# Kernel optimization log

Hardware: AMD Instinct MI355X
Metric: run time of the kernel (lower is better)

The kernel has to match this reference:

```python
import jax, jax.numpy as jnp
import numpy as np


def _attention(v, W, static_hidden, dec_hidden):
    # static_hidden: [B,N,H], dec_hidden: [B,1,H], v: [1,1,H], W: [1,H,2H]
    hidden = jnp.concatenate(
        [static_hidden, jnp.broadcast_to(dec_hidden, static_hidden.shape)], axis=2
    )  # [B,N,2H]
    e = jnp.tanh(jnp.einsum('bnk,hk->bnh', hidden, W[0]))  # W @ hidden^T, done row-wise
    scores = jnp.einsum('bnh,h->bn', e, v[0, 0])  # [B,N]
    return jax.nn.softmax(scores, axis=1)[:, None, :]  # [B,1,N]


def _gru_step(x, h, w_ih, w_hh, b_ih, b_hh):
    # x: [B,H] input, h: [B,H] prev hidden; PyTorch gate order: r | z | n
    gx = x @ w_ih.T + b_ih  # [B,3H]
    gh = h @ w_hh.T + b_hh  # [B,3H]
    H = h.shape[-1]
    r = jax.nn.sigmoid(gx[:, :H] + gh[:, :H])
    z = jax.nn.sigmoid(gx[:, H:2 * H] + gh[:, H:2 * H])
    n = jnp.tanh(gx[:, 2 * H:] + r * gh[:, 2 * H:])
    return (1.0 - z) * n + z * h


def _pointer_scores(v, W, static_hidden, context, state_embedding):
    # energy = cat(static, context, state_emb) -> [B,N,3H]
    energy = jnp.concatenate(
        [static_hidden,
         jnp.broadcast_to(context, static_hidden.shape),
         jnp.broadcast_to(state_embedding, static_hidden.shape)], axis=2)
    e = jnp.tanh(jnp.einsum('bnk,hk->bnh', energy, W[0]))  # [B,N,H]
    return jnp.einsum('bnh,h->bn', e, v[0, 0])  # [B,N]


def setup_inputs() -> dict:
    key = jax.random.key(0)
    B, N, H = 128, 512, 512
    ks = jax.random.split(key, 16)
    s = 0.05
    return {
        'static_hidden': jax.random.normal(ks[0], (B, N, H), jnp.float32),
        'state_embedding': jax.random.normal(ks[1], (B, 1, H), jnp.float32),
        'decoder_hidden': jax.random.normal(ks[2], (B, 1, H), jnp.float32),
        'target_hidden': jax.random.normal(ks[3], (B, 1, H), jnp.float32),
        'last_hh': jax.random.normal(ks[4], (1, B, H), jnp.float32),
        # Pointer params (note: target branch of the original reuses self.v/self.W)
        'ptr_v': jax.random.normal(ks[5], (1, 1, H), jnp.float32) * s,
        'ptr_W': jax.random.normal(ks[6], (1, H, 3 * H), jnp.float32) * s,
        # encoder attention params
        'enc_v': jax.random.normal(ks[7], (1, 1, H), jnp.float32) * s,
        'enc_W': jax.random.normal(ks[8], (1, H, 2 * H), jnp.float32) * s,
        # target attention params
        'tgt_v': jax.random.normal(ks[9], (1, 1, H), jnp.float32) * s,
        'tgt_W': jax.random.normal(ks[10], (1, H, 2 * H), jnp.float32) * s,
        # GRU (single layer) params
        'gru_w_ih': jax.random.normal(ks[11], (3 * H, H), jnp.float32) * s,
        'gru_w_hh': jax.random.normal(ks[12], (3 * H, H), jnp.float32) * s,
        'gru_b_ih': jax.random.normal(ks[13], (3 * H,), jnp.float32) * s,
        'gru_b_hh': jax.random.normal(ks[14], (3 * H,), jnp.float32) * s,
    }


def reference(static_hidden, state_embedding, decoder_hidden, target_hidden, last_hh,
              ptr_v, ptr_W, enc_v, enc_W, tgt_v, tgt_W,
              gru_w_ih, gru_w_hh, gru_b_ih, gru_b_hh):
    # GRU over seq len 1 (batch_first); dropout layers are identity (eval mode)
    h_new = _gru_step(decoder_hidden[:, 0, :], last_hh[0], gru_w_ih, gru_w_hh, gru_b_ih, gru_b_hh)
    rnn_out = h_new[:, None, :]          # [B,1,H]
    new_last_hh = h_new[None]            # [1,B,H]

    # encoder attention + context
    enc_attn = _attention(enc_v, enc_W, static_hidden, rnn_out)   # [B,1,N]
    context = jnp.matmul(enc_attn, static_hidden)                 # [B,1,H]
    probs = _pointer_scores(ptr_v, ptr_W, static_hidden, context, state_embedding)

    # target attention + context (original reuses self.v/self.W for scoring)
    tgt_attn = _attention(tgt_v, tgt_W, static_hidden, target_hidden)
    context_t = jnp.matmul(tgt_attn, static_hidden)
    probs_target = _pointer_scores(ptr_v, ptr_W, static_hidden, context_t, state_embedding)

    probs = 5.0 * probs + probs_target
    return (probs, new_last_hh)
```

## Files before the change

### kernel.cpp

```cpp
#include <hip/hip_runtime.h>
#include <math.h>

#define B 128
#define N 512
#define H 512

typedef __attribute__((ext_vector_type(8))) short short8;
typedef __attribute__((ext_vector_type(4))) float floatx4;

typedef const __attribute__((address_space(1))) unsigned int* gas_t;
typedef __attribute__((address_space(3))) unsigned int* las_t;

__device__ __forceinline__ void gl16(const void* g, void* l){
    __builtin_amdgcn_global_load_lds((gas_t)g, (las_t)l, 16, 0, 0);
}

__device__ __forceinline__ float sigmoidf_(float x){ return 1.0f/(1.0f+__expf(-x)); }

__device__ __forceinline__ float fast_tanh(float x){
    float t = __expf(-2.0f*fabsf(x));
    float r = __fdividef(1.0f - t, 1.0f + t);
    return copysignf(r, x);
}

__device__ __forceinline__ unsigned f2bf1(float f){
    unsigned u = __float_as_uint(f);
    u += 0x7FFFu + ((u>>16)&1u);
    return u>>16;
}
__device__ __forceinline__ unsigned pk2(float a, float b){
    return f2bf1(a) | (f2bf1(b)<<16);
}

__global__ __launch_bounds__(256) void k_cast_all(
    const float* __restrict__ encW, const float* __restrict__ tgtW,
    const float* __restrict__ ptrW, const float* __restrict__ wih,
    const float* __restrict__ whh,
    const float* __restrict__ dec, const float* __restrict__ lhh,
    const float* __restrict__ tgt, const float* __restrict__ sem,
    const float* __restrict__ A,
    unsigned short* __restrict__ We_s, unsigned short* __restrict__ Wt_s,
    unsigned short* __restrict__ Wp_s, unsigned short* __restrict__ We_d,
    unsigned short* __restrict__ Wt_d, unsigned short* __restrict__ Wp_c,
    unsigned short* __restrict__ Wp_e, unsigned short* __restrict__ Wih_b,
    unsigned short* __restrict__ Whh_b,
    unsigned short* __restrict__ Xbf, unsigned short* __restrict__ Hbf,
    unsigned short* __restrict__ Tbf, unsigned short* __restrict__ Sbf,
    unsigned short* __restrict__ Abf)
{
    int r = blockIdx.x, t = threadIdx.x;
    if (r < 6656){
        const float* src; unsigned short* dst; int pitch, off, row;
        if (r < 512)      { src=encW; dst=We_s; pitch=2*H; off=0;   row=r; }
        else if (r<1024)  { src=tgtW; dst=Wt_s; pitch=2*H; off=0;   row=r-512; }
        else if (r<1536)  { src=ptrW; dst=Wp_s; pitch=3*H; off=0;   row=r-1024; }
// ... 131 lines not shown
            short8 af[4], bg[4];
            #pragma unroll
            for (int i=0;i<4;++i){
                int m = wy*64 + i*16 + li;
                int kb = (ks*4 + quad) ^ (m&7);
                af[i] = *(const short8*)&As[m*64 + kb*8];
            }
            #pragma unroll
            for (int j=0;j<4;++j){
                int h = wx*64 + j*16 + li;
                int kb = (ks*4 + quad) ^ (h&7);
                bg[j] = *(const short8*)&Bs[h*64 + kb*8];
            }
            #pragma unroll
            for (int i=0;i<4;++i)
              #pragma unroll
              for (int j=0;j<4;++j)
                acc[i][j] = __builtin_amdgcn_mfma_f32_16x16x32_bf16(af[i], bg[j], acc[i][j], 0,0,0);
        }
        __syncthreads();
    }
    #pragma unroll
    for (int i=0;i<4;++i)
      #pragma unroll
      for (int j=0;j<4;++j)
        #pragma unroll
        for (int rg=0;rg<4;++rg){
            int m = wy*64 + i*16 + quad*4 + rg;
            int n = wx*64 + j*16 + li;
            C[(size_t)m*ldc + n] = acc[i][j][rg];
        }
}

__global__ __launch_bounds__(256,2) void k_gru_gemm(
    const unsigned short* __restrict__ Xbf, const unsigned short* __restrict__ Hbf,
    const unsigned short* __restrict__ Wih_b, const unsigned short* __restrict__ Whh_b,
    float* __restrict__ gx, float* __restrict__ gh)
{
    int blk = blockIdx.x;
    int mat = blk / 12, nt = blk % 12;
    const unsigned short* Ab = mat ? Hbf : Xbf;
    const unsigned short* Bb = (mat ? Whh_b : Wih_b) + (size_t)nt*128*512;
    float* C = (mat ? gh : gx) + nt*128;
    gemm128_tile(Ab, Bb, C, 3*H);
}

__global__ __launch_bounds__(256) void k_gru_gate(const float* __restrict__ gx,
    const float* __restrict__ gh, const float* __restrict__ lhh,
    const float* __restrict__ bih, const float* __restrict__ bhh,
    float* __restrict__ out_hh, unsigned short* __restrict__ hnew_bf)
{
    int idx = blockIdx.x*256 + threadIdx.x;
    int b = idx >> 9, k = idx & 511;
    const float* gxb = gx + (size_t)b*(3*H);
    const float* ghb = gh + (size_t)b*(3*H);
    float r = sigmoidf_(gxb[k]     + bih[k]     + ghb[k]     + bhh[k]);
    float z = sigmoidf_(gxb[H+k]   + bih[H+k]   + ghb[H+k]   + bhh[H+k]);
    float n = tanhf(gxb[2*H+k] + bih[2*H+k] + r*(ghb[2*H+k] + bhh[2*H+k]));
    float h = (1.f-z)*n + z*lhh[idx];
    out_hh[idx] = h;
    hnew_bf[idx] = (unsigned short)f2bf1(h);
}

__global__ __launch_bounds__(256,2) void k_bias_gemm(
    const unsigned short* __restrict__ HNbf, const unsigned short* __restrict__ Tbf,
    const unsigned short* __restrict__ Sbf,
    const unsigned short* __restrict__ We_d, const unsigned short* __restrict__ Wt_d,
    const unsigned short* __restrict__ Wp_e,
    float* __restrict__ d_enc, float* __restrict__ d_tgt, float* __restrict__ d_se)
{
    int blk = blockIdx.x;
    int mat = blk >> 2, nt = blk & 3;
    const unsigned short* Ab = mat==0 ? HNbf : mat==1 ? Tbf : Sbf;
    const unsigned short* Bb = (mat==0 ? We_d : mat==1 ? Wt_d : Wp_e) + (size_t)nt*128*512;
    float* C = (mat==0 ? d_enc : mat==1 ? d_tgt : d_se) + nt*128;
    gemm128_tile(Ab, Bb, C, H);
}

__global__ __launch_bounds__(256,2) void k_dptr_gemm(
    const float* __restrict__ ctx, const float* __restrict__ ctxt,
    const unsigned short* __restrict__ Wp_c,
    float* __restrict__ d_pe, float* __restrict__ d_pt)
{
    int blk = blockIdx.x;
    int mat = blk >> 2, nt = blk & 3;
    const float* Af = mat ? ctxt : ctx;
    const unsigned short* Bb = Wp_c + (size_t)nt*128*512;
    float* C = (mat ? d_pt : d_pe) + nt*128;
    gemm128_tile_f32A(Af, Bb, C, H);
}

template<bool BF16A>
__global__ __launch_bounds__(256,2) void k_scores_fused(
    const float* __restrict__ Af, const unsigned short* __restrict__ Abf,
    const unsigned short* __restrict__ We, const unsigned short* __restrict__ Wt,
    const float* __restrict__ d_enc, const float* __restrict__ d_tgt,
    const float* __restrict__ enc_v, const float* __restrict__ tgt_v,
    float* __restrict__ sc_e, float* __restrict__ sc_t)
{
    __shared__ __align__(16) unsigned short As[128*64];
    __shared__ __align__(16) unsigned short Be[128*64];
    __shared__ __align__(16) unsigned short Bt[128*64];
    int blk = blockIdx.x;
    int b = blk >> 4; int nt = (blk >> 2) & 3; int ht = blk & 3;
    int n0 = nt*128, hb = ht*128;
    int t = threadIdx.x;
    int lane = t & 63, wave = t >> 6;
    int wy = wave >> 1, wx = wave & 1;
    int li = lane & 15, quad = lane >> 4;

    floatx4 acc_e[4][4], acc_t[4][4];
    #pragma unroll
    for (int i=0;i<4;++i)
      #pragma unroll
      for (int j=0;j<4;++j){ acc_e[i][j]=(floatx4)(0.0f); acc_t[i][j]=(floatx4)(0.0f); }

    for (int kt=0; kt<8; ++kt){
        int k0 = kt*64;
        #pragma unroll
        for (int c=0;c<4;++c){
            int s = c*256 + t;
            int row = s >> 3;
            int kb = (s & 7) ^ (row & 7);
            if constexpr (BF16A){
                gl16(&Abf[(size_t)(b*N+n0+row)*H + k0 + kb*8], &As[(size_t)s*8]);
            } else {
                const float* src = Af + (size_t)(b*N+n0+row)*H + k0 + kb*8;
                float4 lo = *(const float4*)src;
                float4 hi = *(const float4*)(src+4);
                uint4 p;
                p.x = pk2(lo.x,lo.y); p.y = pk2(lo.z,lo.w);
                p.z = pk2(hi.x,hi.y); p.w = pk2(hi.z,hi.w);
                *(uint4*)&As[(size_t)s*8] = p;
            }
            gl16(&We[(size_t)(hb+row)*H + k0 + kb*8], &Be[(size_t)s*8]);
            gl16(&Wt[(size_t)(hb+row)*H + k0 + kb*8], &Bt[(size_t)s*8]);
        }
        __syncthreads();
        #pragma unroll
        for (int ks=0;ks<2;++ks){
            short8 af[4], be[4], bt[4];
            #pragma unroll
            for (int i=0;i<4;++i){
                int m = wy*64 + i*16 + li;
                int kb = (ks*4 + quad) ^ (m&7);
                af[i] = *(const short8*)&As[m*64 + kb*8];
            }
            #pragma unroll
            for (int j=0;j<4;++j){
                int h = wx*64 + j*16 + li;
                int kb = (ks*4 + quad) ^ (h&7);
                be[j] = *(const short8*)&Be[h*64 + kb*8];
                bt[j] = *(const short8*)&Bt[h*64 + kb*8];
            }
            #pragma unroll
            for (int i=0;i<4;++i)
              #pragma unroll
              for (int j=0;j<4;++j){
                acc_e[i][j] = __builtin_amdgcn_mfma_f32_16x16x32_bf16(af[i], be[j], acc_e[i][j], 0,0,0);
                acc_t[i][j] = __builtin_amdgcn_mfma_f32_16x16x32_bf16(af[i], bt[j], acc_t[i][j], 0,0,0);
              }
        }
        __syncthreads();
    }
    float nse[4][4], nst[4][4];
    #pragma unroll
    for (int i=0;i<4;++i)
      #pragma unroll
      for (int rg=0;rg<4;++rg){ nse[i][rg]=0.f; nst[i][rg]=0.f; }
    #pragma unroll
    for (int j=0;j<4;++j){
        int hm = hb + wx*64 + j*16 + li;
        float dje = d_enc[b*H+hm], vje = enc_v[hm];
        float djt = d_tgt[b*H+hm], vjt = tgt_v[hm];
        #pragma unroll
        for (int i=0;i<4;++i)
          #pragma unroll
          for (int rg=0;rg<4;++rg){
            nse[i][rg] += vje * fast_tanh(acc_e[i][j][rg] + dje);
            nst[i][rg] += vjt * fast_tanh(acc_t[i][j][rg] + djt);
          }
    }
    #pragma unroll
    for (int off=1; off<16; off<<=1)
      #pragma unroll
      for (int i=0;i<4;++i)
        #pragma unroll
        for (int rg=0;rg<4;++rg){
          nse[i][rg] += __shfl_xor(nse[i][rg], off);
          nst[i][rg] += __shfl_xor(nst[i][rg], off);
        }
    if (li==0){
        #pragma unroll
        for (int i=0;i<4;++i)
          #pragma unroll
          for (int rg=0;rg<4;++rg){
            atomicAdd(&sc_e[b*N + n0 + wy*64 + i*16 + quad*4 + rg], nse[i][rg]);
            atomicAdd(&sc_t[b*N + n0 + wy*64 + i*16 + quad*4 + rg], nst[i][rg]);
          }
    }
}

__global__ __launch_bounds__(256) void k_softmax(const float* __restrict__ sc_e,
    const float* __restrict__ sc_t, float* __restrict__ w_e, float* __restrict__ w_t)
{
    __shared__ float buf[256];
    int b = blockIdx.x, t = threadIdx.x;
    float x0 = sc_e[b*N+t], x1 = sc_e[b*N+t+256];
    float m = fmaxf(x0,x1);
    buf[t]=m; __syncthreads();
    for (int s2=128;s2>0;s2>>=1){ if(t<s2) buf[t]=fmaxf(buf[t],buf[t+s2]); __syncthreads(); }
    m = buf[0]; __syncthreads();
    float e0 = __expf(x0-m), e1 = __expf(x1-m);
    buf[t]=e0+e1; __syncthreads();
    for (int s2=128;s2>0;s2>>=1){ if(t<s2) buf[t]+=buf[t+s2]; __syncthreads(); }
    float inv = 1.0f/buf[0]; __syncthreads();
    w_e[b*N+t]=e0*inv; w_e[b*N+t+256]=e1*inv;
    x0 = sc_t[b*N+t]; x1 = sc_t[b*N+t+256];
    m = fmaxf(x0,x1);
    buf[t]=m; __syncthreads();
    for (int s2=128;s2>0;s2>>=1){ if(t<s2) buf[t]=fmaxf(buf[t],buf[t+s2]); __syncthreads(); }
    m = buf[0]; __syncthreads();
    e0 = __expf(x0-m); e1 = __expf(x1-m);
    buf[t]=e0+e1; __syncthreads();
    for (int s2=128;s2>0;s2>>=1){ if(t<s2) buf[t]+=buf[t+s2]; __syncthreads(); }
    inv = 1.0f/buf[0];
    w_t[b*N+t]=e0*inv; w_t[b*N+t+256]=e1*inv;
}

__global__ __launch_bounds__(256) void k_context_bf16(const unsigned short* __restrict__ Abf,
    const float* __restrict__ w_e, const float* __restrict__ w_t,
    float* __restrict__ ctx, float* __restrict__ ctxt)
{
    __shared__ float we[64], wt[64];
    int b = blockIdx.x >> 3, c = blockIdx.x & 7, t = threadIdx.x;
    int n0 = c*64;
    if (t < 64){ we[t]=w_e[b*N+n0+t]; wt[t]=w_t[b*N+n0+t]; }
    __syncthreads();
    float ae0=0.f, ae1=0.f, at0=0.f, at1=0.f;
    for (int n=0;n<64;++n){
        unsigned u = *(const unsigned*)&Abf[(size_t)(b*N+n0+n)*H + 2*t];
        float lo = __uint_as_float(u<<16);
        float hi = __uint_as_float(u & 0xFFFF0000u);
        float e = we[n], g = wt[n];
        ae0 += e*lo; ae1 += e*hi; at0 += g*lo; at1 += g*hi;
    }
    atomicAdd(&ctx[b*H+2*t],   ae0); atomicAdd(&ctx[b*H+2*t+1],  ae1);
    atomicAdd(&ctxt[b*H+2*t],  at0); atomicAdd(&ctxt[b*H+2*t+1], at1);
}

__global__ __launch_bounds__(256) void k_context(const float* __restrict__ A,
    const float* __restrict__ w_e, const float* __restrict__ w_t,
    float* __restrict__ ctx, float* __restrict__ ctxt)
{
    __shared__ float we[128], wt[128];
    int b = blockIdx.x >> 2, c = blockIdx.x & 3, t = threadIdx.x;
    int n0 = c*128;
    if (t < 128){ we[t]=w_e[b*N+n0+t]; wt[t]=w_t[b*N+n0+t]; }
    __syncthreads();
    float ae0=0.f, ae1=0.f, at0=0.f, at1=0.f;
    for (int n=0;n<128;++n){
        const float* ar = A + (size_t)(b*N + n0 + n)*H;
        float a0 = ar[t], a1 = ar[t+256];
        ae0 += we[n]*a0; ae1 += we[n]*a1;
        at0 += wt[n]*a0; at1 += wt[n]*a1;
    }
    atomicAdd(&ctx[b*H+t],      ae0); atomicAdd(&ctx[b*H+t+256],  ae1);
    atomicAdd(&ctxt[b*H+t],     at0); atomicAdd(&ctxt[b*H+t+256], at1);
}

template<bool BF16A>
__global__ __launch_bounds__(256,2) void k_probs_mfma(
    const float* __restrict__ Af, const unsigned short* __restrict__ Abf,
    const unsigned short* __restrict__ Wp,
    const float* __restrict__ d_pe, const float* __restrict__ d_pt,
    const float* __restrict__ d_se,
    const float* __restrict__ ptr_v, float* __restrict__ probs)
{
    __shared__ __align__(16) unsigned short As[128*64];
    __shared__ __align__(16) unsigned short Bs[128*64];
    int blk = blockIdx.x;
    int b = blk >> 4; int nt = (blk >> 2) & 3; int ht = blk & 3;
    int n0 = nt*128, hb = ht*128;

    int t = threadIdx.x;
    int lane = t & 63, wave = t >> 6;
    int wy = wave >> 1, wx = wave & 1;
    int li = lane & 15, quad = lane >> 4;

    floatx4 acc[4][4];
    #pragma unroll
    for (int i=0;i<4;++i)
      #pragma unroll
      for (int j=0;j<4;++j) acc[i][j] = (floatx4)(0.0f);

    for (int kt=0; kt<8; ++kt){
        int k0 = kt*64;
        #pragma unroll
        for (int c=0;c<4;++c){
            int s = c*256 + t;
            int row = s >> 3;
            int kb = (s & 7) ^ (row & 7);
            if constexpr (BF16A){
                gl16(&Abf[(size_t)(b*N+n0+row)*H + k0 + kb*8], &As[(size_t)s*8]);
            } else {
                const float* src = Af + (size_t)(b*N+n0+row)*H + k0 + kb*8;
                float4 lo = *(const float4*)src;
                float4 hi = *(const float4*)(src+4);
                uint4 p;
                p.x = pk2(lo.x,lo.y); p.y = pk2(lo.z,lo.w);
                p.z = pk2(hi.x,hi.y); p.w = pk2(hi.z,hi.w);
                *(uint4*)&As[(size_t)s*8] = p;
            }
            gl16(&Wp[(size_t)(hb+row)*H + k0 + kb*8], &Bs[(size_t)s*8]);
        }
        __syncthreads();
        #pragma unroll
        for (int ks=0;ks<2;++ks){
            short8 af[4], bg[4];
            #pragma unroll
            for (int i=0;i<4;++i){
                int m = wy*64 + i*16 + li;
                int kb = (ks*4 + quad) ^ (m&7);
                af[i] = *(const short8*)&As[m*64 + kb*8];
            }
            #pragma unroll
            for (int j=0;j<4;++j){
                int h = wx*64 + j*16 + li;
                int kb = (ks*4 + quad) ^ (h&7);
                bg[j] = *(const short8*)&Bs[h*64 + kb*8];
            }
            #pragma unroll
            for (int i=0;i<4;++i)
              #pragma unroll
              for (int j=0;j<4;++j)
                acc[i][j] = __builtin_amdgcn_mfma_f32_16x16x32_bf16(af[i], bg[j], acc[i][j], 0,0,0);
        }
        __syncthreads();
    }
    float nsum[4][4];
    #pragma unroll
    for (int i=0;i<4;++i){ nsum[i][0]=0.f;nsum[i][1]=0.f;nsum[i][2]=0.f;nsum[i][3]=0.f; }
    #pragma unroll
    for (int j=0;j<4;++j){
        int hm = hb + wx*64 + j*16 + li;
        float se = d_se[b*H + hm];
        float de = d_pe[b*H + hm] + se;
        float dt = d_pt[b*H + hm] + se;
        float vj = ptr_v[hm];
        #pragma unroll
        for (int i=0;i<4;++i)
          #pragma unroll
          for (int rg=0;rg<4;++rg){
            float s = acc[i][j][rg];
            nsum[i][rg] += vj * (5.0f*fast_tanh(s + de) + fast_tanh(s + dt));
          }
    }
    #pragma unroll
    for (int off=1; off<16; off<<=1)
      #pragma unroll
      for (int i=0;i<4;++i)
        #pragma unroll
        for (int rg=0;rg<4;++rg)
          nsum[i][rg] += __shfl_xor(nsum[i][rg], off);
    if (li==0){
        #pragma unroll
        for (int i=0;i<4;++i)
          #pragma unroll
          for (int rg=0;rg<4;++rg)
            atomicAdd(&probs[b*N + n0 + wy*64 + i*16 + quad*4 + rg], nsum[i][rg]);
    }
}
// ... 1 lines not shown
extern "C" void kernel_launch(void* const* d_in, const int* in_sizes, int n_in,
                              void* d_out, int out_size, void* d_ws, size_t ws_size,
                              hipStream_t stream)
{
    (void)in_sizes; (void)n_in; (void)out_size;
    const float* A    = (const float*)d_in[0];
    const float* sem  = (const float*)d_in[1];
    const float* dec  = (const float*)d_in[2];
    const float* tgt  = (const float*)d_in[3];
    const float* lhh  = (const float*)d_in[4];
    const float* ptrv = (const float*)d_in[5];
    const float* ptrW = (const float*)d_in[6];
    const float* encv = (const float*)d_in[7];
    const float* encW = (const float*)d_in[8];
    const float* tgtv = (const float*)d_in[9];
    const float* tgtW = (const float*)d_in[10];
    const float* wih  = (const float*)d_in[11];
    const float* whh  = (const float*)d_in[12];
    const float* bih  = (const float*)d_in[13];
    const float* bhh  = (const float*)d_in[14];

    float* probs_out = (float*)d_out;
    float* hh_out    = (float*)d_out + B*N;

    float* ws = (float*)d_ws;
    const size_t S = (size_t)B*H;
    float* d_enc = ws;
    float* d_tgt = ws + S;
    float* d_se  = ws + 2*S;
    float* sc_e  = ws + 3*S;
    float* sc_t  = ws + 4*S;
    float* ctx   = ws + 5*S;
    float* ctxt  = ws + 6*S;
    float* w_e   = ws + 7*S;
    float* w_t   = ws + 8*S;
    float* d_pe  = ws + 9*S;
    float* d_pt  = ws + 10*S;
    float* gx    = ws + 11*S;
    float* gh    = ws + 14*S;
    unsigned short* bfb  = (unsigned short*)(ws + 17*S);
    const size_t WH = (size_t)H*H;
    const size_t WG = (size_t)3*H*H;
    unsigned short* We_s  = bfb;
    unsigned short* Wt_s  = We_s + WH;
    unsigned short* Wp_s  = Wt_s + WH;
    unsigned short* We_d  = Wp_s + WH;
    unsigned short* Wt_d  = We_d + WH;
    unsigned short* Wp_c  = Wt_d + WH;
    unsigned short* Wp_e  = Wp_c + WH;
    unsigned short* Wih_b = Wp_e + WH;
    unsigned short* Whh_b = Wih_b + WG;
    unsigned short* Xbf   = Whh_b + WG;
    unsigned short* Hbf   = Xbf + S;
    unsigned short* Tbf   = Hbf + S;
    unsigned short* Sbf   = Tbf + S;
    unsigned short* HNbf  = Sbf + S;
    unsigned short* Abf   = HNbf + S;

    const size_t need_full = 17*S*sizeof(float)
        + (7*WH + 2*WG + 5*S + (size_t)B*N*H) * sizeof(unsigned short);
    const bool big = ws_size >= need_full;

    hipMemsetAsync(sc_e, 0, 4*S*sizeof(float), stream);
    hipMemsetAsync(probs_out, 0, (size_t)B*N*sizeof(float), stream);

    int castA_blocks = big ? (int)(((size_t)B*N*H)/(256*8)) : 0;
    k_cast_all<<<6784 + castA_blocks, 256, 0, stream>>>(encW, tgtW, ptrW, wih, whh,
        dec, lhh, tgt, sem, A,
        We_s, Wt_s, Wp_s, We_d, Wt_d, Wp_c, Wp_e, Wih_b, Whh_b,
        Xbf, Hbf, Tbf, Sbf, Abf);

    k_gru_gemm<<<24, 256, 0, stream>>>(Xbf, Hbf, Wih_b, Whh_b, gx, gh);
    k_gru_gate<<<256, 256, 0, stream>>>(gx, gh, lhh, bih, bhh, hh_out, HNbf);
    k_bias_gemm<<<12, 256, 0, stream>>>(HNbf, Tbf, Sbf, We_d, Wt_d, Wp_e, d_enc, d_tgt, d_se);

    if (big)
        k_scores_fused<true ><<<2048, 256, 0, stream>>>(A, Abf, We_s, Wt_s, d_enc, d_tgt, encv, tgtv, sc_e, sc_t);
    else
        k_scores_fused<false><<<2048, 256, 0, stream>>>(A, Abf, We_s, Wt_s, d_enc, d_tgt, encv, tgtv, sc_e, sc_t);
    k_softmax<<<B, 256, 0, stream>>>(sc_e, sc_t, w_e, w_t);
    if (big)
        k_context_bf16<<<B*8, 256, 0, stream>>>(Abf, w_e, w_t, ctx, ctxt);
    else
        k_context<<<B*4, 256, 0, stream>>>(A, w_e, w_t, ctx, ctxt);

    k_dptr_gemm<<<8, 256, 0, stream>>>(ctx, ctxt, Wp_c, d_pe, d_pt);

    if (big)
        k_probs_mfma<true ><<<2048, 256, 0, stream>>>(A, Abf, Wp_s, d_pe, d_pt, d_se, ptrv, probs_out);
    else
        k_probs_mfma<false><<<2048, 256, 0, stream>>>(A, Abf, Wp_s, d_pe, d_pt, d_se, ptrv, probs_out);
}
```

Before: 472.9 us.

## Load MFMA fragments directly from global, use rational tanh, merge bias GEMMs

The two large MFMA kernels (scores and pointer probs) no longer stage A and W tiles through LDS with barriers. Each lane now loads its bf16 fragments straight from global memory and the k-loop is fully unrolled, which removes the LDS traffic and syncs but depends on L1/L2 for reuse across waves. fast_tanh becomes a clamped Padé rational approximation in place of an exp plus divide. The target and state bias GEMMs move into the GRU GEMM launch, since they do not depend on the GRU output, leaving a smaller separate launch for the encoder bias.

```diff
diff --git a/kernel.cpp b/kernel.cpp
--- a/kernel.cpp
+++ b/kernel.cpp
@@ -18,9 +18,11 @@
 __device__ __forceinline__ float sigmoidf_(float x){ return 1.0f/(1.0f+__expf(-x)); }
 
 __device__ __forceinline__ float fast_tanh(float x){
-    float t = __expf(-2.0f*fabsf(x));
-    float r = __fdividef(1.0f - t, 1.0f + t);
-    return copysignf(r, x);
+    float xc = fminf(fmaxf(x, -4.97f), 4.97f);
+    float x2 = xc*xc;
+    float num = xc * (135135.0f + x2*(17325.0f + x2*(378.0f + x2)));
+    float den = 135135.0f + x2*(62370.0f + x2*(3150.0f + x2*28.0f));
+    return __fdividef(num, den);
 }
 
 __device__ __forceinline__ unsigned f2bf1(float f){
@@ -218,17 +220,28 @@
         }
 }
 
-__global__ __launch_bounds__(256,2) void k_gru_gemm(
+__global__ __launch_bounds__(256,2) void k_pre(
     const unsigned short* __restrict__ Xbf, const unsigned short* __restrict__ Hbf,
+    const unsigned short* __restrict__ Tbf, const unsigned short* __restrict__ Sbf,
     const unsigned short* __restrict__ Wih_b, const unsigned short* __restrict__ Whh_b,
-    float* __restrict__ gx, float* __restrict__ gh)
+    const unsigned short* __restrict__ Wt_d, const unsigned short* __restrict__ Wp_e,
+    float* __restrict__ gx, float* __restrict__ gh,
+    float* __restrict__ d_tgt, float* __restrict__ d_se)
 {
     int blk = blockIdx.x;
-    int mat = blk / 12, nt = blk % 12;
-    const unsigned short* Ab = mat ? Hbf : Xbf;
-    const unsigned short* Bb = (mat ? Whh_b : Wih_b) + (size_t)nt*128*512;
-    float* C = (mat ? gh : gx) + nt*128;
-    gemm128_tile(Ab, Bb, C, 3*H);
+    if (blk < 24){
+        int mat = blk / 12, nt = blk % 12;
+        const unsigned short* Ab = mat ? Hbf : Xbf;
+        const unsigned short* Bb = (mat ? Whh_b : Wih_b) + (size_t)nt*128*512;
+        float* C = (mat ? gh : gx) + nt*128;
+        gemm128_tile(Ab, Bb, C, 3*H);
+    } else if (blk < 28){
+        int nt = blk - 24;
+        gemm128_tile(Tbf, Wt_d + (size_t)nt*128*512, d_tgt + nt*128, H);
+    } else {
+        int nt = blk - 28;
+        gemm128_tile(Sbf, Wp_e + (size_t)nt*128*512, d_se + nt*128, H);
+    }
 }
 
 __global__ __launch_bounds__(256) void k_gru_gate(const float* __restrict__ gx,
@@ -248,19 +261,12 @@
     hnew_bf[idx] = (unsigned short)f2bf1(h);
 }
 
-__global__ __launch_bounds__(256,2) void k_bias_gemm(
-    const unsigned short* __restrict__ HNbf, const unsigned short* __restrict__ Tbf,
-    const unsigned short* __restrict__ Sbf,
-    const unsigned short* __restrict__ We_d, const unsigned short* __restrict__ Wt_d,
-    const unsigned short* __restrict__ Wp_e,
-    float* __restrict__ d_enc, float* __restrict__ d_tgt, float* __restrict__ d_se)
-{
-    int blk = blockIdx.x;
-    int mat = blk >> 2, nt = blk & 3;
-    const unsigned short* Ab = mat==0 ? HNbf : mat==1 ? Tbf : Sbf;
-    const unsigned short* Bb = (mat==0 ? We_d : mat==1 ? Wt_d : Wp_e) + (size_t)nt*128*512;
-    float* C = (mat==0 ? d_enc : mat==1 ? d_tgt : d_se) + nt*128;
-    gemm128_tile(Ab, Bb, C, H);
+__global__ __launch_bounds__(256,2) void k_bias0(
+    const unsigned short* __restrict__ HNbf, const unsigned short* __restrict__ We_d,
+    float* __restrict__ d_enc)
+{
+    int nt = blockIdx.x;
+    gemm128_tile(HNbf, We_d + (size_t)nt*128*512, d_enc + nt*128, H);
 }
 
 __global__ __launch_bounds__(256,2) void k_dptr_gemm(
@@ -274,6 +280,21 @@
     const unsigned short* Bb = Wp_c + (size_t)nt*128*512;
     float* C = (mat ? d_pt : d_pe) + nt*128;
     gemm128_tile_f32A(Af, Bb, C, H);
+}
+
+template<bool BF16>
+__device__ __forceinline__ short8 load_frag(const unsigned short* pb, const float* pf, int off){
+    if constexpr (BF16){
+        return *(const short8*)(pb + off);
+    } else {
+        float4 lo = *(const float4*)(pf + off);
+        float4 hi = *(const float4*)(pf + off + 4);
+        uint4 p;
+        p.x = pk2(lo.x,lo.y); p.y = pk2(lo.z,lo.w);
+        p.z = pk2(hi.x,hi.y); p.w = pk2(hi.z,hi.w);
+        union { uint4 u; short8 s; } cv; cv.u = p;
+        return cv.s;
+    }
 }
 
 template<bool BF16A>
@@ -284,9 +305,6 @@
     const float* __restrict__ enc_v, const float* __restrict__ tgt_v,
     float* __restrict__ sc_e, float* __restrict__ sc_t)
 {
-    __shared__ __align__(16) unsigned short As[128*64];
-    __shared__ __align__(16) unsigned short Be[128*64];
-    __shared__ __align__(16) unsigned short Bt[128*64];
     int blk = blockIdx.x;
     int b = blk >> 4; int nt = (blk >> 2) & 3; int ht = blk & 3;
     int n0 = nt*128, hb = ht*128;
@@ -295,60 +313,45 @@
     int wy = wave >> 1, wx = wave & 1;
     int li = lane & 15, quad = lane >> 4;
 
+    const unsigned short* pA[4]; const float* pAf[4];
+    #pragma unroll
+    for (int i=0;i<4;++i){
+        size_t r = (size_t)(b*N + n0 + wy*64 + i*16 + li)*H + quad*8;
+        if constexpr (BF16A) pA[i] = Abf + r; else pAf[i] = Af + r;
+    }
+    const unsigned short* pE[4]; const unsigned short* pT[4];
+    #pragma unroll
+    for (int j=0;j<4;++j){
+        size_t r = (size_t)(hb + wx*64 + j*16 + li)*H + quad*8;
+        pE[j] = We + r; pT[j] = Wt + r;
+    }
+
     floatx4 acc_e[4][4], acc_t[4][4];
     #pragma unroll
     for (int i=0;i<4;++i)
       #pragma unroll
       for (int j=0;j<4;++j){ acc_e[i][j]=(floatx4)(0.0f); acc_t[i][j]=(floatx4)(0.0f); }
 
-    for (int kt=0; kt<8; ++kt){
-        int k0 = kt*64;
-        #pragma unroll
-        for (int c=0;c<4;++c){
-            int s = c*256 + t;
-            int row = s >> 3;
-            int kb = (s & 7) ^ (row & 7);
-            if constexpr (BF16A){
-                gl16(&Abf[(size_t)(b*N+n0+row)*H + k0 + kb*8], &As[(size_t)s*8]);
-            } else {
-                const float* src = Af + (size_t)(b*N+n0+row)*H + k0 + kb*8;
-                float4 lo = *(const float4*)src;
-                float4 hi = *(const float4*)(src+4);
-                uint4 p;
-                p.x = pk2(lo.x,lo.y); p.y = pk2(lo.z,lo.w);
-                p.z = pk2(hi.x,hi.y); p.w = pk2(hi.z,hi.w);
-                *(uint4*)&As[(size_t)s*8] = p;
-            }
-            gl16(&We[(size_t)(hb+row)*H + k0 + kb*8], &Be[(size_t)s*8]);
-            gl16(&Wt[(size_t)(hb+row)*H + k0 + kb*8], &Bt[(size_t)s*8]);
-        }
-        __syncthreads();
-        #pragma unroll
-        for (int ks=0;ks<2;++ks){
-            short8 af[4], be[4], bt[4];
-            #pragma unroll
-            for (int i=0;i<4;++i){
-                int m = wy*64 + i*16 + li;
-                int kb = (ks*4 + quad) ^ (m&7);
-                af[i] = *(const short8*)&As[m*64 + kb*8];
-            }
-            #pragma unroll
-            for (int j=0;j<4;++j){
-                int h = wx*64 + j*16 + li;
-                int kb = (ks*4 + quad) ^ (h&7);
-                be[j] = *(const short8*)&Be[h*64 + kb*8];
-                bt[j] = *(const short8*)&Bt[h*64 + kb*8];
-            }
-            #pragma unroll
-            for (int i=0;i<4;++i)
-              #pragma unroll
-              for (int j=0;j<4;++j){
-                acc_e[i][j] = __builtin_amdgcn_mfma_f32_16x16x32_bf16(af[i], be[j], acc_e[i][j], 0,0,0);
-                acc_t[i][j] = __builtin_amdgcn_mfma_f32_16x16x32_bf16(af[i], bt[j], acc_t[i][j], 0,0,0);
-              }
-        }
-        __syncthreads();
-    }
+    #pragma unroll
+    for (int kk=0; kk<16; ++kk){
+        int off = kk*32;
+        short8 af[4], be[4], bt[4];
+        #pragma unroll
+        for (int i=0;i<4;++i) af[i] = load_frag<BF16A>(pA[i], pAf[i], off);
+        #pragma unroll
+        for (int j=0;j<4;++j){
+            be[j] = *(const short8*)(pE[j] + off);
+            bt[j] = *(const short8*)(pT[j] + off);
+        }
+        #pragma unroll
+        for (int i=0;i<4;++i)
+          #pragma unroll
+          for (int j=0;j<4;++j){
+            acc_e[i][j] = __builtin_amdgcn_mfma_f32_16x16x32_bf16(af[i], be[j], acc_e[i][j], 0,0,0);
+            acc_t[i][j] = __builtin_amdgcn_mfma_f32_16x16x32_bf16(af[i], bt[j], acc_t[i][j], 0,0,0);
+          }
+    }
+
     float nse[4][4], nst[4][4];
     #pragma unroll
     for (int i=0;i<4;++i)
@@ -463,67 +466,46 @@
     const float* __restrict__ d_se,
     const float* __restrict__ ptr_v, float* __restrict__ probs)
 {
-    __shared__ __align__(16) unsigned short As[128*64];
-    __shared__ __align__(16) unsigned short Bs[128*64];
     int blk = blockIdx.x;
     int b = blk >> 4; int nt = (blk >> 2) & 3; int ht = blk & 3;
     int n0 = nt*128, hb = ht*128;
-
     int t = threadIdx.x;
     int lane = t & 63, wave = t >> 6;
     int wy = wave >> 1, wx = wave & 1;
     int li = lane & 15, quad = lane >> 4;
 
+    const unsigned short* pA[4]; const float* pAf[4];
+    #pragma unroll
+    for (int i=0;i<4;++i){
+        size_t r = (size_t)(b*N + n0 + wy*64 + i*16 + li)*H + quad*8;
+        if constexpr (BF16A) pA[i] = Abf + r; else pAf[i] = Af + r;
+    }
+    const unsigned short* pB[4];
+    #pragma unroll
+    for (int j=0;j<4;++j)
+        pB[j] = Wp + (size_t)(hb + wx*64 + j*16 + li)*H + quad*8;
+
     floatx4 acc[4][4];
     #pragma unroll
     for (int i=0;i<4;++i)
       #pragma unroll
       for (int j=0;j<4;++j) acc[i][j] = (floatx4)(0.0f);
 
-    for (int kt=0; kt<8; ++kt){
-        int k0 = kt*64;
-        #pragma unroll
-        for (int c=0;c<4;++c){
-            int s = c*256 + t;
-            int row = s >> 3;
-            int kb = (s & 7) ^ (row & 7);
-            if constexpr (BF16A){
-                gl16(&Abf[(size_t)(b*N+n0+row)*H + k0 + kb*8], &As[(size_t)s*8]);
-            } else {
-                const float* src = Af + (size_t)(b*N+n0+row)*H + k0 + kb*8;
-                float4 lo = *(const float4*)src;
-                float4 hi = *(const float4*)(src+4);
-                uint4 p;
-                p.x = pk2(lo.x,lo.y); p.y = pk2(lo.z,lo.w);
-                p.z = pk2(hi.x,hi.y); p.w = pk2(hi.z,hi.w);
-                *(uint4*)&As[(size_t)s*8] = p;
-            }
-            gl16(&Wp[(size_t)(hb+row)*H + k0 + kb*8], &Bs[(size_t)s*8]);
-        }
-        __syncthreads();
-        #pragma unroll
-        for (int ks=0;ks<2;++ks){
-            short8 af[4], bg[4];
-            #pragma unroll
-            for (int i=0;i<4;++i){
-                int m = wy*64 + i*16 + li;
-                int kb = (ks*4 + quad) ^ (m&7);
-                af[i] = *(const short8*)&As[m*64 + kb*8];
-            }
-            #pragma unroll
-            for (int j=0;j<4;++j){
-                int h = wx*64 + j*16 + li;
-                int kb = (ks*4 + quad) ^ (h&7);
-                bg[j] = *(const short8*)&Bs[h*64 + kb*8];
-            }
-            #pragma unroll
-            for (int i=0;i<4;++i)
-              #pragma unroll
-              for (int j=0;j<4;++j)
-                acc[i][j] = __builtin_amdgcn_mfma_f32_16x16x32_bf16(af[i], bg[j], acc[i][j], 0,0,0);
-        }
-        __syncthreads();
-    }
+    #pragma unroll
+    for (int kk=0; kk<16; ++kk){
+        int off = kk*32;
+        short8 af[4], bg[4];
+        #pragma unroll
+        for (int i=0;i<4;++i) af[i] = load_frag<BF16A>(pA[i], pAf[i], off);
+        #pragma unroll
+        for (int j=0;j<4;++j) bg[j] = *(const short8*)(pB[j] + off);
+        #pragma unroll
+        for (int i=0;i<4;++i)
+          #pragma unroll
+          for (int j=0;j<4;++j)
+            acc[i][j] = __builtin_amdgcn_mfma_f32_16x16x32_bf16(af[i], bg[j], acc[i][j], 0,0,0);
+    }
+
     float nsum[4][4];
     #pragma unroll
     for (int i=0;i<4;++i){ nsum[i][0]=0.f;nsum[i][1]=0.f;nsum[i][2]=0.f;nsum[i][3]=0.f; }
@@ -629,9 +611,10 @@
         We_s, Wt_s, Wp_s, We_d, Wt_d, Wp_c, Wp_e, Wih_b, Whh_b,
         Xbf, Hbf, Tbf, Sbf, Abf);
 
-    k_gru_gemm<<<24, 256, 0, stream>>>(Xbf, Hbf, Wih_b, Whh_b, gx, gh);
+    k_pre<<<32, 256, 0, stream>>>(Xbf, Hbf, Tbf, Sbf, Wih_b, Whh_b, Wt_d, Wp_e,
+        gx, gh, d_tgt, d_se);
     k_gru_gate<<<256, 256, 0, stream>>>(gx, gh, lhh, bih, bhh, hh_out, HNbf);
-    k_bias_gemm<<<12, 256, 0, stream>>>(HNbf, Tbf, Sbf, We_d, Wt_d, Wp_e, d_enc, d_tgt, d_se);
+    k_bias0<<<4, 256, 0, stream>>>(HNbf, We_d, d_enc);
 
     if (big)
         k_scores_fused<true ><<<2048, 256, 0, stream>>>(A, Abf, We_s, Wt_s, d_enc, d_tgt, encv, tgtv, sc_e, sc_t);
```

After: 617.4 us. 30.6% more time.

## Fuse softmax into context, merge bias GEMMs into GRU launch, rational tanh

Applied to the files above, without the earlier changes.

Several changes land together. Fast tanh becomes a clamped Padé rational approximation instead of exp plus divide. The target and state bias GEMMs move into the GRU GEMM launch, so only the encoder bias GEMM still waits for the GRU gate. The standalone softmax kernel is folded into the context kernels, with each block recomputing the softmax of its batch row using wave shuffles. The bf16 MFMA load loops also get precomputed pointer increments for global and LDS addressing. These cut launches, intermediate buffers and address arithmetic, but the softmax is now recomputed redundantly per block and the tanh approximation changes accuracy slightly.

```diff
diff --git a/kernel.cpp b/kernel.cpp
--- a/kernel.cpp
+++ b/kernel.cpp
@@ -18,9 +18,11 @@
 __device__ __forceinline__ float sigmoidf_(float x){ return 1.0f/(1.0f+__expf(-x)); }
 
 __device__ __forceinline__ float fast_tanh(float x){
-    float t = __expf(-2.0f*fabsf(x));
-    float r = __fdividef(1.0f - t, 1.0f + t);
-    return copysignf(r, x);
+    float xc = fminf(fmaxf(x, -4.97f), 4.97f);
+    float x2 = xc*xc;
+    float num = xc * (135135.0f + x2*(17325.0f + x2*(378.0f + x2)));
+    float den = 135135.0f + x2*(62370.0f + x2*(3150.0f + x2*28.0f));
+    return __fdividef(num, den);
 }
 
 __device__ __forceinline__ unsigned f2bf1(float f){
@@ -218,17 +220,28 @@
         }
 }
 
-__global__ __launch_bounds__(256,2) void k_gru_gemm(
+__global__ __launch_bounds__(256,2) void k_pre(
     const unsigned short* __restrict__ Xbf, const unsigned short* __restrict__ Hbf,
+    const unsigned short* __restrict__ Tbf, const unsigned short* __restrict__ Sbf,
     const unsigned short* __restrict__ Wih_b, const unsigned short* __restrict__ Whh_b,
-    float* __restrict__ gx, float* __restrict__ gh)
+    const unsigned short* __restrict__ Wt_d, const unsigned short* __restrict__ Wp_e,
+    float* __restrict__ gx, float* __restrict__ gh,
+    float* __restrict__ d_tgt, float* __restrict__ d_se)
 {
     int blk = blockIdx.x;
-    int mat = blk / 12, nt = blk % 12;
-    const unsigned short* Ab = mat ? Hbf : Xbf;
-    const unsigned short* Bb = (mat ? Whh_b : Wih_b) + (size_t)nt*128*512;
-    float* C = (mat ? gh : gx) + nt*128;
-    gemm128_tile(Ab, Bb, C, 3*H);
+    if (blk < 24){
+        int mat = blk / 12, nt = blk % 12;
+        const unsigned short* Ab = mat ? Hbf : Xbf;
+        const unsigned short* Bb = (mat ? Whh_b : Wih_b) + (size_t)nt*128*512;
+        float* C = (mat ? gh : gx) + nt*128;
+        gemm128_tile(Ab, Bb, C, 3*H);
+    } else if (blk < 28){
+        int nt = blk - 24;
+        gemm128_tile(Tbf, Wt_d + (size_t)nt*128*512, d_tgt + nt*128, H);
+    } else {
+        int nt = blk - 28;
+        gemm128_tile(Sbf, Wp_e + (size_t)nt*128*512, d_se + nt*128, H);
+    }
 }
 
 __global__ __launch_bounds__(256) void k_gru_gate(const float* __restrict__ gx,
@@ -248,19 +261,12 @@
     hnew_bf[idx] = (unsigned short)f2bf1(h);
 }
 
-__global__ __launch_bounds__(256,2) void k_bias_gemm(
-    const unsigned short* __restrict__ HNbf, const unsigned short* __restrict__ Tbf,
-    const unsigned short* __restrict__ Sbf,
-    const unsigned short* __restrict__ We_d, const unsigned short* __restrict__ Wt_d,
-    const unsigned short* __restrict__ Wp_e,
-    float* __restrict__ d_enc, float* __restrict__ d_tgt, float* __restrict__ d_se)
-{
-    int blk = blockIdx.x;
-    int mat = blk >> 2, nt = blk & 3;
-    const unsigned short* Ab = mat==0 ? HNbf : mat==1 ? Tbf : Sbf;
-    const unsigned short* Bb = (mat==0 ? We_d : mat==1 ? Wt_d : Wp_e) + (size_t)nt*128*512;
-    float* C = (mat==0 ? d_enc : mat==1 ? d_tgt : d_se) + nt*128;
-    gemm128_tile(Ab, Bb, C, H);
+__global__ __launch_bounds__(256,2) void k_bias0(
+    const unsigned short* __restrict__ HNbf, const unsigned short* __restrict__ We_d,
+    float* __restrict__ d_enc)
+{
+    int nt = blockIdx.x;
+    gemm128_tile(HNbf, We_d + (size_t)nt*128*512, d_enc + nt*128, H);
 }
 
 __global__ __launch_bounds__(256,2) void k_dptr_gemm(
@@ -301,16 +307,65 @@
       #pragma unroll
       for (int j=0;j<4;++j){ acc_e[i][j]=(floatx4)(0.0f); acc_t[i][j]=(floatx4)(0.0f); }
 
-    for (int kt=0; kt<8; ++kt){
-        int k0 = kt*64;
+    const unsigned short* rA[2]; const unsigned short* rE[2]; const unsigned short* rT[2];
+    #pragma unroll
+    for (int ks=0;ks<2;++ks){
+        int kb = (ks*4 + quad) ^ (li & 7);
+        rA[ks] = &As[(wy*64 + li)*64 + kb*8];
+        rE[ks] = &Be[(wx*64 + li)*64 + kb*8];
+        rT[ks] = &Bt[(wx*64 + li)*64 + kb*8];
+    }
+
+    if constexpr (BF16A){
+        int rs = t >> 3;
+        int kb = (t & 7) ^ (rs & 7);
+        const unsigned short* gA[4]; const unsigned short* gE[4]; const unsigned short* gT[4];
+        unsigned short* lA[4]; unsigned short* lE[4]; unsigned short* lT[4];
         #pragma unroll
         for (int c=0;c<4;++c){
+            int row = c*32 + rs;
+            gA[c] = Abf + (size_t)(b*N + n0 + row)*H + kb*8;
+            gE[c] = We  + (size_t)(hb + row)*H + kb*8;
+            gT[c] = Wt  + (size_t)(hb + row)*H + kb*8;
             int s = c*256 + t;
-            int row = s >> 3;
-            int kb = (s & 7) ^ (row & 7);
-            if constexpr (BF16A){
-                gl16(&Abf[(size_t)(b*N+n0+row)*H + k0 + kb*8], &As[(size_t)s*8]);
-            } else {
+            lA[c] = &As[(size_t)s*8]; lE[c] = &Be[(size_t)s*8]; lT[c] = &Bt[(size_t)s*8];
+        }
+        for (int kt=0; kt<8; ++kt){
+            #pragma unroll
+            for (int c=0;c<4;++c){
+                gl16(gA[c], lA[c]); gA[c] += 64;
+                gl16(gE[c], lE[c]); gE[c] += 64;
+                gl16(gT[c], lT[c]); gT[c] += 64;
+            }
+            __syncthreads();
+            #pragma unroll
+            for (int ks=0;ks<2;++ks){
+                short8 af[4], be[4], bt[4];
+                #pragma unroll
+                for (int i=0;i<4;++i) af[i] = *(const short8*)(rA[ks] + i*1024);
+                #pragma unroll
+                for (int j=0;j<4;++j){
+                    be[j] = *(const short8*)(rE[ks] + j*1024);
+                    bt[j] = *(const short8*)(rT[ks] + j*1024);
+                }
+                #pragma unroll
+                for (int i=0;i<4;++i)
+                  #pragma unroll
+                  for (int j=0;j<4;++j){
+                    acc_e[i][j] = __builtin_amdgcn_mfma_f32_16x16x32_bf16(af[i], be[j], acc_e[i][j], 0,0,0);
+                    acc_t[i][j] = __builtin_amdgcn_mfma_f32_16x16x32_bf16(af[i], bt[j], acc_t[i][j], 0,0,0);
+                  }
+            }
+            __syncthreads();
+        }
+    } else {
+        for (int kt=0; kt<8; ++kt){
+            int k0 = kt*64;
+            #pragma unroll
+            for (int c=0;c<4;++c){
+                int s = c*256 + t;
+                int row = s >> 3;
+                int kb = (s & 7) ^ (row & 7);
                 const float* src = Af + (size_t)(b*N+n0+row)*H + k0 + kb*8;
                 float4 lo = *(const float4*)src;
                 float4 hi = *(const float4*)(src+4);
@@ -318,37 +373,32 @@
                 p.x = pk2(lo.x,lo.y); p.y = pk2(lo.z,lo.w);
                 p.z = pk2(hi.x,hi.y); p.w = pk2(hi.z,hi.w);
                 *(uint4*)&As[(size_t)s*8] = p;
-            }
-            gl16(&We[(size_t)(hb+row)*H + k0 + kb*8], &Be[(size_t)s*8]);
-            gl16(&Wt[(size_t)(hb+row)*H + k0 + kb*8], &Bt[(size_t)s*8]);
-        }
-        __syncthreads();
-        #pragma unroll
-        for (int ks=0;ks<2;++ks){
-            short8 af[4], be[4], bt[4];
-            #pragma unroll
-            for (int i=0;i<4;++i){
-                int m = wy*64 + i*16 + li;
-                int kb = (ks*4 + quad) ^ (m&7);
-                af[i] = *(const short8*)&As[m*64 + kb*8];
-            }
-            #pragma unroll
-            for (int j=0;j<4;++j){
-                int h = wx*64 + j*16 + li;
-                int kb = (ks*4 + quad) ^ (h&7);
-                be[j] = *(const short8*)&Be[h*64 + kb*8];
-                bt[j] = *(const short8*)&Bt[h*64 + kb*8];
-            }
-            #pragma unroll
-            for (int i=0;i<4;++i)
-              #pragma unroll
-              for (int j=0;j<4;++j){
-                acc_e[i][j] = __builtin_amdgcn_mfma_f32_16x16x32_bf16(af[i], be[j], acc_e[i][j], 0,0,0);
-                acc_t[i][j] = __builtin_amdgcn_mfma_f32_16x16x32_bf16(af[i], bt[j], acc_t[i][j], 0,0,0);
-              }
-        }
-        __syncthreads();
-    }
+                gl16(&We[(size_t)(hb+row)*H + k0 + kb*8], &Be[(size_t)s*8]);
+                gl16(&Wt[(size_t)(hb+row)*H + k0 + kb*8], &Bt[(size_t)s*8]);
+            }
+            __syncthreads();
+            #pragma unroll
+            for (int ks=0;ks<2;++ks){
+                short8 af[4], be[4], bt[4];
+                #pragma unroll
+                for (int i=0;i<4;++i) af[i] = *(const short8*)(rA[ks] + i*1024);
+                #pragma unroll
+                for (int j=0;j<4;++j){
+                    be[j] = *(const short8*)(rE[ks] + j*1024);
+                    bt[j] = *(const short8*)(rT[ks] + j*1024);
+                }
+                #pragma unroll
+                for (int i=0;i<4;++i)
+                  #pragma unroll
+                  for (int j=0;j<4;++j){
+                    acc_e[i][j] = __builtin_amdgcn_mfma_f32_16x16x32_bf16(af[i], be[j], acc_e[i][j], 0,0,0);
+                    acc_t[i][j] = __builtin_amdgcn_mfma_f32_16x16x32_bf16(af[i], bt[j], acc_t[i][j], 0,0,0);
+                  }
+            }
+            __syncthreads();
+        }
+    }
+
     float nse[4][4], nst[4][4];
     #pragma unroll
     for (int i=0;i<4;++i)
@@ -387,69 +437,98 @@
     }
 }
 
-__global__ __launch_bounds__(256) void k_softmax(const float* __restrict__ sc_e,
-    const float* __restrict__ sc_t, float* __restrict__ w_e, float* __restrict__ w_t)
-{
-    __shared__ float buf[256];
-    int b = blockIdx.x, t = threadIdx.x;
-    float x0 = sc_e[b*N+t], x1 = sc_e[b*N+t+256];
-    float m = fmaxf(x0,x1);
-    buf[t]=m; __syncthreads();
-    for (int s2=128;s2>0;s2>>=1){ if(t<s2) buf[t]=fmaxf(buf[t],buf[t+s2]); __syncthreads(); }
-    m = buf[0]; __syncthreads();
-    float e0 = __expf(x0-m), e1 = __expf(x1-m);
-    buf[t]=e0+e1; __syncthreads();
-    for (int s2=128;s2>0;s2>>=1){ if(t<s2) buf[t]+=buf[t+s2]; __syncthreads(); }
-    float inv = 1.0f/buf[0]; __syncthreads();
-    w_e[b*N+t]=e0*inv; w_e[b*N+t+256]=e1*inv;
-    x0 = sc_t[b*N+t]; x1 = sc_t[b*N+t+256];
-    m = fmaxf(x0,x1);
-    buf[t]=m; __syncthreads();
-    for (int s2=128;s2>0;s2>>=1){ if(t<s2) buf[t]=fmaxf(buf[t],buf[t+s2]); __syncthreads(); }
-    m = buf[0]; __syncthreads();
-    e0 = __expf(x0-m); e1 = __expf(x1-m);
-    buf[t]=e0+e1; __syncthreads();
-    for (int s2=128;s2>0;s2>>=1){ if(t<s2) buf[t]+=buf[t+s2]; __syncthreads(); }
-    inv = 1.0f/buf[0];
-    w_t[b*N+t]=e0*inv; w_t[b*N+t+256]=e1*inv;
-}
-
-__global__ __launch_bounds__(256) void k_context_bf16(const unsigned short* __restrict__ Abf,
-    const float* __restrict__ w_e, const float* __restrict__ w_t,
+__global__ __launch_bounds__(256) void k_ctx_sm(const unsigned short* __restrict__ Abf,
+    const float* __restrict__ sc_e, const float* __restrict__ sc_t,
     float* __restrict__ ctx, float* __restrict__ ctxt)
 {
-    __shared__ float we[64], wt[64];
+    __shared__ float wse[512], wst[512];
+    __shared__ float red[16];
     int b = blockIdx.x >> 3, c = blockIdx.x & 7, t = threadIdx.x;
+    int lane = t & 63, wave = t >> 6;
+    float e0 = sc_e[b*N+t], e1 = sc_e[b*N+256+t];
+    float t0 = sc_t[b*N+t], t1 = sc_t[b*N+256+t];
+    float me = fmaxf(e0,e1), mt = fmaxf(t0,t1);
+    #pragma unroll
+    for (int off=1; off<64; off<<=1){
+        me = fmaxf(me, __shfl_xor(me, off));
+        mt = fmaxf(mt, __shfl_xor(mt, off));
+    }
+    if (lane==0){ red[wave]=me; red[4+wave]=mt; }
+    __syncthreads();
+    me = fmaxf(fmaxf(red[0],red[1]), fmaxf(red[2],red[3]));
+    mt = fmaxf(fmaxf(red[4],red[5]), fmaxf(red[6],red[7]));
+    float ee0 = __expf(e0-me), ee1 = __expf(e1-me);
+    float et0 = __expf(t0-mt), et1 = __expf(t1-mt);
+    float se = ee0+ee1, st = et0+et1;
+    #pragma unroll
+    for (int off=1; off<64; off<<=1){
+        se += __shfl_xor(se, off);
+        st += __shfl_xor(st, off);
+    }
+    __syncthreads();
+    if (lane==0){ red[8+wave]=se; red[12+wave]=st; }
+    __syncthreads();
+    float inve = 1.0f/(red[8]+red[9]+red[10]+red[11]);
+    float invt = 1.0f/(red[12]+red[13]+red[14]+red[15]);
+    wse[t]=ee0*inve; wse[256+t]=ee1*inve;
+    wst[t]=et0*invt; wst[256+t]=et1*invt;
+    __syncthreads();
     int n0 = c*64;
-    if (t < 64){ we[t]=w_e[b*N+n0+t]; wt[t]=w_t[b*N+n0+t]; }
-    __syncthreads();
     float ae0=0.f, ae1=0.f, at0=0.f, at1=0.f;
     for (int n=0;n<64;++n){
         unsigned u = *(const unsigned*)&Abf[(size_t)(b*N+n0+n)*H + 2*t];
         float lo = __uint_as_float(u<<16);
         float hi = __uint_as_float(u & 0xFFFF0000u);
-        float e = we[n], g = wt[n];
+        float e = wse[n0+n], g = wst[n0+n];
         ae0 += e*lo; ae1 += e*hi; at0 += g*lo; at1 += g*hi;
     }
     atomicAdd(&ctx[b*H+2*t],   ae0); atomicAdd(&ctx[b*H+2*t+1],  ae1);
     atomicAdd(&ctxt[b*H+2*t],  at0); atomicAdd(&ctxt[b*H+2*t+1], at1);
 }
 
-__global__ __launch_bounds__(256) void k_context(const float* __restrict__ A,
-    const float* __restrict__ w_e, const float* __restrict__ w_t,
+__global__ __launch_bounds__(256) void k_ctx_sm_f32(const float* __restrict__ A,
+    const float* __restrict__ sc_e, const float* __restrict__ sc_t,
     float* __restrict__ ctx, float* __restrict__ ctxt)
 {
-    __shared__ float we[128], wt[128];
+    __shared__ float wse[512], wst[512];
+    __shared__ float red[16];
     int b = blockIdx.x >> 2, c = blockIdx.x & 3, t = threadIdx.x;
+    int lane = t & 63, wave = t >> 6;
+    float e0 = sc_e[b*N+t], e1 = sc_e[b*N+256+t];
+    float t0 = sc_t[b*N+t], t1 = sc_t[b*N+256+t];
+    float me = fmaxf(e0,e1), mt = fmaxf(t0,t1);
+    #pragma unroll
+    for (int off=1; off<64; off<<=1){
+        me = fmaxf(me, __shfl_xor(me, off));
+        mt = fmaxf(mt, __shfl_xor(mt, off));
+    }
+    if (lane==0){ red[wave]=me; red[4+wave]=mt; }
+    __syncthreads();
+    me = fmaxf(fmaxf(red[0],red[1]), fmaxf(red[2],red[3]));
+    mt = fmaxf(fmaxf(red[4],red[5]), fmaxf(red[6],red[7]));
+    float ee0 = __expf(e0-me), ee1 = __expf(e1-me);
+    float et0 = __expf(t0-mt), et1 = __expf(t1-mt);
+    float se = ee0+ee1, st = et0+et1;
+    #pragma unroll
+    for (int off=1; off<64; off<<=1){
+        se += __shfl_xor(se, off);
+        st += __shfl_xor(st, off);
+    }
+    __syncthreads();
+    if (lane==0){ red[8+wave]=se; red[12+wave]=st; }
+    __syncthreads();
+    float inve = 1.0f/(red[8]+red[9]+red[10]+red[11]);
+    float invt = 1.0f/(red[12]+red[13]+red[14]+red[15]);
+    wse[t]=ee0*inve; wse[256+t]=ee1*inve;
+    wst[t]=et0*invt; wst[256+t]=et1*invt;
+    __syncthreads();
     int n0 = c*128;
-    if (t < 128){ we[t]=w_e[b*N+n0+t]; wt[t]=w_t[b*N+n0+t]; }
-    __syncthreads();
     float ae0=0.f, ae1=0.f, at0=0.f, at1=0.f;
     for (int n=0;n<128;++n){
         const float* ar = A + (size_t)(b*N + n0 + n)*H;
         float a0 = ar[t], a1 = ar[t+256];
-        ae0 += we[n]*a0; ae1 += we[n]*a1;
-        at0 += wt[n]*a0; at1 += wt[n]*a1;
+        float e = wse[n0+n], g = wst[n0+n];
+        ae0 += e*a0; ae1 += e*a1; at0 += g*a0; at1 += g*a1;
     }
     atomicAdd(&ctx[b*H+t],      ae0); atomicAdd(&ctx[b*H+t+256],  ae1);
     atomicAdd(&ctxt[b*H+t],     at0); atomicAdd(&ctxt[b*H+t+256], at1);
@@ -468,7 +547,6 @@
     int blk = blockIdx.x;
     int b = blk >> 4; int nt = (blk >> 2) & 3; int ht = blk & 3;
     int n0 = nt*128, hb = ht*128;
-
     int t = threadIdx.x;
     int lane = t & 63, wave = t >> 6;
     int wy = wave >> 1, wx = wave & 1;
@@ -480,16 +558,57 @@
       #pragma unroll
       for (int j=0;j<4;++j) acc[i][j] = (floatx4)(0.0f);
 
-    for (int kt=0; kt<8; ++kt){
-        int k0 = kt*64;
+    const unsigned short* rA[2]; const unsigned short* rB[2];
+    #pragma unroll
+    for (int ks=0;ks<2;++ks){
+        int kb = (ks*4 + quad) ^ (li & 7);
+        rA[ks] = &As[(wy*64 + li)*64 + kb*8];
+        rB[ks] = &Bs[(wx*64 + li)*64 + kb*8];
+    }
+
+    if constexpr (BF16A){
+        int rs = t >> 3;
+        int kb = (t & 7) ^ (rs & 7);
+        const unsigned short* gA[4]; const unsigned short* gB[4];
+        unsigned short* lA[4]; unsigned short* lB[4];
         #pragma unroll
         for (int c=0;c<4;++c){
+            int row = c*32 + rs;
+            gA[c] = Abf + (size_t)(b*N + n0 + row)*H + kb*8;
+            gB[c] = Wp  + (size_t)(hb + row)*H + kb*8;
             int s = c*256 + t;
-            int row = s >> 3;
-            int kb = (s & 7) ^ (row & 7);
-            if constexpr (BF16A){
-                gl16(&Abf[(size_t)(b*N+n0+row)*H + k0 + kb*8], &As[(size_t)s*8]);
-            } else {
+            lA[c] = &As[(size_t)s*8]; lB[c] = &Bs[(size_t)s*8];
+        }
+        for (int kt=0; kt<8; ++kt){
+            #pragma unroll
+            for (int c=0;c<4;++c){
+                gl16(gA[c], lA[c]); gA[c] += 64;
+                gl16(gB[c], lB[c]); gB[c] += 64;
+            }
+            __syncthreads();
+            #pragma unroll
+            for (int ks=0;ks<2;++ks){
+                short8 af[4], bg[4];
+                #pragma unroll
+                for (int i=0;i<4;++i) af[i] = *(const short8*)(rA[ks] + i*1024);
+                #pragma unroll
+                for (int j=0;j<4;++j) bg[j] = *(const short8*)(rB[ks] + j*1024);
+                #pragma unroll
+                for (int i=0;i<4;++i)
+                  #pragma unroll
+                  for (int j=0;j<4;++j)
+                    acc[i][j] = __builtin_amdgcn_mfma_f32_16x16x32_bf16(af[i], bg[j], acc[i][j], 0,0,0);
+            }
+            __syncthreads();
+        }
+    } else {
+        for (int kt=0; kt<8; ++kt){
+            int k0 = kt*64;
+            #pragma unroll
+            for (int c=0;c<4;++c){
+                int s = c*256 + t;
+                int row = s >> 3;
+                int kb = (s & 7) ^ (row & 7);
                 const float* src = Af + (size_t)(b*N+n0+row)*H + k0 + kb*8;
                 float4 lo = *(const float4*)src;
                 float4 hi = *(const float4*)(src+4);
@@ -497,33 +616,26 @@
                 p.x = pk2(lo.x,lo.y); p.y = pk2(lo.z,lo.w);
                 p.z = pk2(hi.x,hi.y); p.w = pk2(hi.z,hi.w);
                 *(uint4*)&As[(size_t)s*8] = p;
-            }
-            gl16(&Wp[(size_t)(hb+row)*H + k0 + kb*8], &Bs[(size_t)s*8]);
-        }
-        __syncthreads();
-        #pragma unroll
-        for (int ks=0;ks<2;++ks){
-            short8 af[4], bg[4];
-            #pragma unroll
-            for (int i=0;i<4;++i){
-                int m = wy*64 + i*16 + li;
-                int kb = (ks*4 + quad) ^ (m&7);
-                af[i] = *(const short8*)&As[m*64 + kb*8];
-            }
-            #pragma unroll
-            for (int j=0;j<4;++j){
-                int h = wx*64 + j*16 + li;
-                int kb = (ks*4 + quad) ^ (h&7);
-                bg[j] = *(const short8*)&Bs[h*64 + kb*8];
-            }
-            #pragma unroll
-            for (int i=0;i<4;++i)
-              #pragma unroll
-              for (int j=0;j<4;++j)
-                acc[i][j] = __builtin_amdgcn_mfma_f32_16x16x32_bf16(af[i], bg[j], acc[i][j], 0,0,0);
-        }
-        __syncthreads();
-    }
+                gl16(&Wp[(size_t)(hb+row)*H + k0 + kb*8], &Bs[(size_t)s*8]);
+            }
+            __syncthreads();
+            #pragma unroll
+            for (int ks=0;ks<2;++ks){
+                short8 af[4], bg[4];
+                #pragma unroll
+                for (int i=0;i<4;++i) af[i] = *(const short8*)(rA[ks] + i*1024);
+                #pragma unroll
+                for (int j=0;j<4;++j) bg[j] = *(const short8*)(rB[ks] + j*1024);
+                #pragma unroll
+                for (int i=0;i<4;++i)
+                  #pragma unroll
+                  for (int j=0;j<4;++j)
+                    acc[i][j] = __builtin_amdgcn_mfma_f32_16x16x32_bf16(af[i], bg[j], acc[i][j], 0,0,0);
+            }
+            __syncthreads();
+        }
+    }
+
     float nsum[4][4];
     #pragma unroll
     for (int i=0;i<4;++i){ nsum[i][0]=0.f;nsum[i][1]=0.f;nsum[i][2]=0.f;nsum[i][3]=0.f; }
@@ -591,13 +703,11 @@
     float* sc_t  = ws + 4*S;
     float* ctx   = ws + 5*S;
     float* ctxt  = ws + 6*S;
-    float* w_e   = ws + 7*S;
-    float* w_t   = ws + 8*S;
-    float* d_pe  = ws + 9*S;
-    float* d_pt  = ws + 10*S;
-    float* gx    = ws + 11*S;
-    float* gh    = ws + 14*S;
-    unsigned short* bfb  = (unsigned short*)(ws + 17*S);
+    float* d_pe  = ws + 7*S;
+    float* d_pt  = ws + 8*S;
+    float* gx    = ws + 9*S;
+    float* gh    = ws + 12*S;
+    unsigned short* bfb  = (unsigned short*)(ws + 15*S);
     const size_t WH = (size_t)H*H;
     const size_t WG = (size_t)3*H*H;
     unsigned short* We_s  = bfb;
@@ -616,7 +726,7 @@
     unsigned short* HNbf  = Sbf + S;
     unsigned short* Abf   = HNbf + S;
 
-    const size_t need_full = 17*S*sizeof(float)
+    const size_t need_full = 15*S*sizeof(float)
         + (7*WH + 2*WG + 5*S + (size_t)B*N*H) * sizeof(unsigned short);
     const bool big = ws_size >= need_full;
 
@@ -629,19 +739,20 @@
         We_s, Wt_s, Wp_s, We_d, Wt_d, Wp_c, Wp_e, Wih_b, Whh_b,
         Xbf, Hbf, Tbf, Sbf, Abf);
 
-    k_gru_gemm<<<24, 256, 0, stream>>>(Xbf, Hbf, Wih_b, Whh_b, gx, gh);
+    k_pre<<<32, 256, 0, stream>>>(Xbf, Hbf, Tbf, Sbf, Wih_b, Whh_b, Wt_d, Wp_e,
+        gx, gh, d_tgt, d_se);
     k_gru_gate<<<256, 256, 0, stream>>>(gx, gh, lhh, bih, bhh, hh_out, HNbf);
-    k_bias_gemm<<<12, 256, 0, stream>>>(HNbf, Tbf, Sbf, We_d, Wt_d, Wp_e, d_enc, d_tgt, d_se);
+    k_bias0<<<4, 256, 0, stream>>>(HNbf, We_d, d_enc);
 
     if (big)
         k_scores_fused<true ><<<2048, 256, 0, stream>>>(A, Abf, We_s, Wt_s, d_enc, d_tgt, encv, tgtv, sc_e, sc_t);
     else
         k_scores_fused<false><<<2048, 256, 0, stream>>>(A, Abf, We_s, Wt_s, d_enc, d_tgt, encv, tgtv, sc_e, sc_t);
-    k_softmax<<<B, 256, 0, stream>>>(sc_e, sc_t, w_e, w_t);
+
     if (big)
-        k_context_bf16<<<B*8, 256, 0, stream>>>(Abf, w_e, w_t, ctx, ctxt);
+        k_ctx_sm<<<B*8, 256, 0, stream>>>(Abf, sc_e, sc_t, ctx, ctxt);
     else
-        k_context<<<B*4, 256, 0, stream>>>(A, w_e, w_t, ctx, ctxt);
+        k_ctx_sm_f32<<<B*4, 256, 0, stream>>>(A, sc_e, sc_t, ctx, ctxt);
 
     k_dptr_gemm<<<8, 256, 0, stream>>>(ctx, ctxt, Wp_c, d_pe, d_pt);
 
```

After: 473.6 us. No clear change (+0.1%).
